# Kernel tuning notes

Hardware: AMD Instinct MI355X
Metric: run time of the kernel (lower is better)

Reference implementation:

```python
import jax, jax.numpy as jnp
import numpy as np

N_NODES = 100000
N_EDGES = 1600000
IN_FEATS = 128
N_HIDDEN = 128
N_CLASSES = 16
INIT_EPS = 0.0
N_GIN_LAYERS = 4  # n_layers + 1


def setup_inputs() -> dict:
    key = jax.random.key(0)
    ks = jax.random.split(key, 16)
    features = jax.random.normal(ks[0], (N_NODES, IN_FEATS), dtype=jnp.float32)
    src = jax.random.randint(ks[1], (N_EDGES,), 0, N_NODES, dtype=jnp.int64)
    dst = jax.random.randint(ks[2], (N_EDGES,), 0, N_NODES, dtype=jnp.int64)
    def linear(k, fin, fout):
        bound = 1.0 / np.sqrt(fin)
        kw, kb = jax.random.split(k)
        W = jax.random.uniform(kw, (fin, fout), jnp.float32, -bound, bound)
        b = jax.random.uniform(kb, (fout,), jnp.float32, -bound, bound)
        return W, b
    W0, b0 = linear(ks[3], IN_FEATS, N_HIDDEN)
    W1, b1 = linear(ks[4], N_HIDDEN, N_HIDDEN)
    W2, b2 = linear(ks[5], N_HIDDEN, N_HIDDEN)
    W3, b3 = linear(ks[6], N_HIDDEN, N_CLASSES)
    eps = jnp.full((N_GIN_LAYERS,), INIT_EPS, dtype=jnp.float32)
    return {"features": features, "src": src, "dst": dst,
            "W0": W0, "b0": b0, "W1": W1, "b1": b1,
            "W2": W2, "b2": b2, "W3": W3, "b3": b3, "eps": eps}


def _mean_agg(h, src, dst, inv_deg):
    # gather neighbor features along edges, sum into dst, divide by in-degree
    agg = jax.ops.segment_sum(h[src], dst, num_segments=N_NODES)
    return agg * inv_deg


def _gin_layer(h, src, dst, inv_deg, eps, W, b, relu):
    z = (1.0 + eps) * h + _mean_agg(h, src, dst, inv_deg)
    out = z @ W + b  # Dropout is identity in eval mode
    return jax.nn.relu(out) if relu else out


def reference(features, src, dst, W0, b0, W1, b1, W2, b2, W3, b3, eps):
    deg = jax.ops.segment_sum(jnp.ones((src.shape[0],), features.dtype), dst,
                              num_segments=N_NODES)
    inv_deg = (1.0 / jnp.maximum(deg, 1.0))[:, None]
    h = _gin_layer(features, src, dst, inv_deg, eps[0], W0, b0, relu=True)
    h = _gin_layer(h, src, dst, inv_deg, eps[1], W1, b1, relu=True)
    h = _gin_layer(h, src, dst, inv_deg, eps[2], W2, b2, relu=True)
    h = _gin_layer(h, src, dst, inv_deg, eps[3], W3, b3, relu=False)
    return h
```

## Files before the change

### kernel.cpp

```cpp
#include <hip/hip_runtime.h>

#define NODES 100000
#define EDGES 1600000
#define FEATS 128
#define NCLS  16

#define BSH    6
#define BNODES 64
#define NB     ((NODES + BNODES - 1) / BNODES)
#define CHUNK  8192
#define NBLK   ((EDGES + CHUNK - 1) / CHUNK)
#define NHIST  (NB * NBLK)
#define BCAP   2048
#define NGRP   ((NODES + 15) / 16)

typedef unsigned int  u32;
typedef unsigned short u16;
typedef unsigned long long u64;
typedef __attribute__((ext_vector_type(8))) short short8;
typedef __attribute__((ext_vector_type(4))) float f32x4;

__device__ __forceinline__ float b2f(u16 v){ return __uint_as_float(((u32)v)<<16); }
__device__ __forceinline__ u16 f2b(float f){
  u32 u = __float_as_uint(f);
  u += 0x7fffu + ((u>>16)&1u);
  return (u16)(u>>16);
}
__device__ __forceinline__ float blo(u32 p){ return __uint_as_float(p<<16); }
__device__ __forceinline__ float bhi(u32 p){ return __uint_as_float(p & 0xffff0000u); }

__device__ __forceinline__ void gload16(const u16* g, u16* l){
  __builtin_amdgcn_global_load_lds(
      (const __attribute__((address_space(1))) u32*)g,
      (__attribute__((address_space(3))) u32*)l, 16, 0, 0);
}


__global__ __launch_bounds__(256) void pA_k(const int* __restrict__ dst,
                                            int* __restrict__ gh, int E){
  __shared__ int hist[NB];
  int t = threadIdx.x, blk = blockIdx.x;
  for (int j = t; j < NB; j += 256) hist[j] = 0;
  __syncthreads();
  int e0 = blk*CHUNK, e1 = e0 + CHUNK; if (e1 > E) e1 = E;
  for (int e = e0 + t; e < e1; e += 256) atomicAdd(&hist[dst[e] >> BSH], 1);
  __syncthreads();
  for (int j = t; j < NB; j += 256) gh[j*NBLK + blk] = hist[j];
}


__global__ __launch_bounds__(256) void scan1_k(const int* __restrict__ in, int* __restrict__ out,
                                               int* __restrict__ bsum, int n){
  __shared__ int sh[256];
  int t = threadIdx.x;
  int base = blockIdx.x*2048 + t*8;
  int v[8]; int s = 0;
  #pragma unroll
  for (int j=0;j<8;++j) v[j] = (base+j < n) ? in[base+j] : 0;
  #pragma unroll
  for (int j=0;j<8;++j){ int tmp = v[j]; v[j] = s; s += tmp; }
  sh[t] = s; __syncthreads();
  for (int off=1; off<256; off<<=1){
    int x = (t>=off) ? sh[t-off] : 0;
    __syncthreads();
    sh[t] += x;
    __syncthreads();
  }
  int excl = sh[t] - s;
  #pragma unroll
  for (int j=0;j<8;++j) if (base+j < n) out[base+j] = excl + v[j];
  if (t == 255) bsum[blockIdx.x] = sh[255];
}

__global__ __launch_bounds__(256) void scan2_k(const int* __restrict__ bsum,
                                               int* __restrict__ boff, int nb){
  __shared__ int sh[256];
  int t = threadIdx.x;
  int v = (t < nb) ? bsum[t] : 0;
  sh[t] = v; __syncthreads();
  for (int off=1; off<256; off<<=1){
    int x = (t>=off) ? sh[t-off] : 0;
    __syncthreads();
    sh[t] += x;
    __syncthreads();
  }
  if (t < nb) boff[t] = sh[t] - v;
}

__global__ void scan3_k(int* __restrict__ gscan, const int* __restrict__ boff,
                        int* __restrict__ bstart, int n){
  int i = blockIdx.x*256 + threadIdx.x;
  if (i < n){
    int v = gscan[i] + boff[i>>11];
    gscan[i] = v;
    if (i % NBLK == 0) bstart[i / NBLK] = v;
    if (i == 0) bstart[NB] = EDGES;
  }
}


__global__ __launch_bounds__(256) void pC_k(const int* __restrict__ src,
    const int* __restrict__ dst, const int* __restrict__ gscan,
    u32* __restrict__ elist, int E){
  __shared__ int A[NB];
  __shared__ int B[NB];
  __shared__ int sp[256];
  __shared__ u32 pay[CHUNK];
  __shared__ u16 bkt[CHUNK];
  int t = threadIdx.x, blk = blockIdx.x;
  for (int j = t; j < NB; j += 256) A[j] = 0;
  __syncthreads();
  int e0 = blk*CHUNK, e1 = e0 + CHUNK; if (e1 > E) e1 = E;
  int cnt = e1 - e0;
  for (int e = e0 + t; e < e1; e += 256) atomicAdd(&A[dst[e] >> BSH], 1);
  __syncthreads();
  {
    int base = t*7;
    int cv[7]; int s = 0;
    #pragma unroll
    for (int j=0;j<7;++j){ int idx = base+j; cv[j] = (idx < NB) ? A[idx] : 0; s += cv[j]; }
    sp[t] = s; __syncthreads();
    for (int off=1; off<256; off<<=1){
      int x = (t>=off) ? sp[t-off] : 0;
      __syncthreads();
      sp[t] += x;
      __syncthreads();
    }
    int run = sp[t] - s;
    #pragma unroll
    for (int j=0;j<7;++j){
      int idx = base+j;
      if (idx < NB){ A[idx] = run; B[idx] = run; run += cv[j]; }
    }
  }
  __syncthreads();
  for (int j = t; j < NB; j += 256) A[j] = gscan[j*NBLK + blk] - A[j];
  __syncthreads();
  for (int e = e0 + t; e < e1; e += 256){
    int d = dst[e];
    int b = d >> BSH;
    u32 w = ((u32)(d & (BNODES-1)) << 17) | (u32)src[e];
    int r = atomicAdd(&B[b], 1);
    pay[r] = w; bkt[r] = (u16)b;
  }
  __syncthreads();
  for (int i = t; i < cnt; i += 256){
    int b = bkt[i];
    elist[i + A[b]] = pay[i];
  }
}


__global__ __launch_bounds__(256) void csr_k(u32* __restrict__ elist,
    const int* __restrict__ bstart, int* __restrict__ offs, int* __restrict__ degs,
    float* __restrict__ invd, int M){
  __shared__ int hist[BNODES];
  __shared__ int pos[BNODES];
  __shared__ u32 buf[BCAP];
  __shared__ u32 buf2[BCAP];
  int b = blockIdx.x, t = threadIdx.x;
  if (b == 0 && t == 0) offs[M] = EDGES;
  if (t < BNODES) hist[t] = 0;
  __syncthreads();
  int s0 = bstart[b];
  int cnt = bstart[b+1] - s0; if (cnt > BCAP) cnt = BCAP;
  u32* el = elist + s0;
  for (int e = t; e < cnt; e += 256){
    u32 w = el[e];
    buf[e] = w;
    atomicAdd(&hist[w>>17], 1);
  }
  __syncthreads();
  if (t < BNODES){
    int v = hist[t];
    int s = v;
    for (int off = 1; off < BNODES; off <<= 1){
      int x = __shfl_up(s, off);
      if (t >= off) s += x;
    }
    int excl = s - v;
    pos[t] = excl;
    int node = b*BNODES + t;
    if (node < M){
      offs[node] = s0 + excl;
      degs[node] = v;
      invd[node] = 1.f / fmaxf((float)v, 1.f);
    }
  }
  __syncthreads();
  for (int e = t; e < cnt; e += 256){
    u32 w = buf[e];
    int p = atomicAdd(&pos[w>>17], 1);
    buf2[p] = w;
  }
  __syncthreads();
  for (int e = t; e < cnt; e += 256) el[e] = buf2[e];
}


__global__ void convf_k(const float* __restrict__ in, u16* __restrict__ o, int n4){
  int i = blockIdx.x*256 + threadIdx.x;
  if (i < n4){
    float4 x = ((const float4*)in)[i];
    ushort4 r;
    r.x = f2b(x.x); r.y = f2b(x.y); r.z = f2b(x.z); r.w = f2b(x.w);
    ((ushort4*)o)[i] = r;
  }
}

__global__ void convw_k(const float* __restrict__ W, u16* __restrict__ Wt, int Kd, int Nd){
  int i = blockIdx.x*256 + threadIdx.x;
  if (i < Kd*Nd){
    int k = i / Nd, nn = i - k*Nd;
    Wt[nn*Kd + k] = f2b(W[i]);
  }
}


template<int NT>
__global__ __launch_bounds__(256) void gemm_k(const u16* __restrict__ h,
                                              const u16* __restrict__ Wt,
                                              u16* __restrict__ y, int M){
  const int K = FEATS;
  const int N = NT*16;
  int lane = threadIdx.x & 63;
  int wave = threadIdx.x >> 6;
  int m    = lane & 15;
  int quad = lane >> 4;
  int row0 = (blockIdx.x*4 + wave)*16;
  if (row0 >= M) return;
  int rowA = row0 + m; if (rowA > M-1) rowA = M-1;
  const u16* pa = h + (size_t)rowA*K + quad*8;

  f32x4 acc[NT];
  #pragma unroll
  for (int j=0;j<NT;++j) acc[j] = (f32x4){0.f,0.f,0.f,0.f};

  #pragma unroll
  for (int kk=0; kk<K; kk+=32){
    short8 a = *(const short8*)(pa + kk);
    #pragma unroll
    for (int j=0;j<NT;++j){
      short8 b = *(const short8*)(Wt + (size_t)(j*16 + m)*K + kk + quad*8);
      acc[j] = __builtin_amdgcn_mfma_f32_16x16x32_bf16(a, b, acc[j], 0, 0, 0);
    }
  }

  #pragma unroll
  for (int j=0;j<NT;++j){
    #pragma unroll
    for (int r=0;r<4;++r){
      int row = row0 + quad*4 + r;
      if (row < M) y[(size_t)row*N + j*16 + m] = f2b(acc[j][r]);
    }
  }
}


#define TRRD(dstv, lit) asm volatile("ds_read_b64_tr_b16 %0, %1 offset:" lit \
                                     : "=v"(dstv) : "v"(trb2))

__global__ __launch_bounds__(256) void aggM_k(const u16* __restrict__ y,
    const u32* __restrict__ el, const int* __restrict__ offs,
    const float* __restrict__ invd, const float* __restrict__ bias,
    const float* __restrict__ epsv, int ei, u16* __restrict__ hout){
  __shared__ __align__(128) u16 ybuf[4][4096];
  int lane = threadIdx.x & 63;
  int wave = threadIdx.x >> 6;
  int grp = blockIdx.x*4 + wave;
  if (grp >= NGRP) return;
  int v0 = grp << 4;
  int m    = lane & 15;
  int quad = lane >> 4;
  u32 tgt = (u32)(((grp & 3) << 4) + m);

  u16* lb = &ybuf[wave][0];
  typedef __attribute__((address_space(3))) u16 lds_u16;
  u32 lbaddr = (u32)(size_t)(lds_u16*)lb;
  u32 trb2 = lbaddr + (u32)(quad*2048) + (u32)(m*8);

  int rsel = (lane & 7) >> 1;
  int gcol = ((lane >> 3) << 4) + ((lane & 1) << 3);

  int e0 = offs[v0];
  int e1 = offs[v0 + 16];
  int nstep = (e1 - e0 + 31) >> 5;

  f32x4 acc[8];
  #pragma unroll
  for (int cb=0;cb<8;++cb) acc[cb] = (f32x4){0.f,0.f,0.f,0.f};

  for (int st = 0; st < nstep; ++st){
    int idx = e0 + (st<<5) + (lane & 31);
    u32 w = (idx < e1) ? el[idx] : 0xFFFE0000u;

    #pragma unroll
    for (int i=0;i<8;++i){
      u32 ws = (u32)__shfl((int)w, 4*i + rsel);
      int srow = (int)(ws & 0x1FFFFu);
      gload16(y + ((size_t)srow << 7) + gcol, lb + i*512);
    }

    union { u32 wv[4]; short8 s; } au;
    #pragma unroll
    for (int p=0;p<4;++p){
      u32 w0 = (u32)__shfl((int)w, quad*8 + 2*p);
      u32 w1 = (u32)__shfl((int)w, quad*8 + 2*p + 1);
      au.wv[p] = (((w0>>17) == tgt) ? 0x3F80u : 0u)
               | (((w1>>17) == tgt) ? 0x3F800000u : 0u);
    }

    asm volatile("s_waitcnt vmcnt(0)" ::: "memory");
    __builtin_amdgcn_sched_barrier(0);

    u64 t[16];
    TRRD(t[0],  "0");    TRRD(t[1],  "1024");
    TRRD(t[2],  "128");  TRRD(t[3],  "1152");
    TRRD(t[4],  "256");  TRRD(t[5],  "1280");
    TRRD(t[6],  "384");  TRRD(t[7],  "1408");
    TRRD(t[8],  "512");  TRRD(t[9],  "1536");
    TRRD(t[10], "640");  TRRD(t[11], "1664");
    TRRD(t[12], "768");  TRRD(t[13], "1792");
    TRRD(t[14], "896");  TRRD(t[15], "1920");
    asm volatile("s_waitcnt lgkmcnt(0)" ::: "memory");
    __builtin_amdgcn_sched_barrier(0);

    #pragma unroll
    for (int cb=0;cb<8;++cb){
      union { u64 d[2]; short8 s; } bu;
      bu.d[0] = t[2*cb]; bu.d[1] = t[2*cb+1];
      acc[cb] = __builtin_amdgcn_mfma_f32_16x16x32_bf16(au.s, bu.s, acc[cb], 0, 0, 0);
    }
  }

  float myinv = invd[v0 + m];
  float invr[4];
  #pragma unroll
  for (int r=0;r<4;++r) invr[r] = __shfl(myinv, quad*4 + r);
  float e1s = 1.f + epsv[ei];
  #pragma unroll
  for (int cb=0;cb<8;++cb){
    float bi = bias[cb*16 + m];
    #pragma unroll
    for (int r=0;r<4;++r){
      size_t off = (size_t)(v0 + quad*4 + r)*FEATS + cb*16 + m;
      float self = b2f(y[off]);
      float o = fmaxf(e1s*self + invr[r]*acc[cb][r] + bi, 0.f);
      hout[off] = f2b(o);
    }
  }
}


__global__ __launch_bounds__(256) void aggF2_k(const u16* __restrict__ y,
    const u32* __restrict__ el, const int* __restrict__ offs,
    const int* __restrict__ degs, const float* __restrict__ invd,
    const float* __restrict__ bias, const float* __restrict__ epsv,
    float* __restrict__ out, int M){
  int lane = threadIdx.x & 63;
  int v = blockIdx.x*4 + (threadIdx.x >> 6);
  if (v >= M) return;
  int sub = lane >> 3;
  int f2  = lane & 7;
  const u32* y2 = (const u32*)y;
  int start = offs[v], deg = degs[v];
  float acc0 = 0.f, acc1 = 0.f;
  for (int e = sub; e < deg; e += 8){
    u32 s = el[start + e] & 0x1FFFFu;
    u32 p = y2[(size_t)s*8 + f2];
    acc0 += blo(p); acc1 += bhi(p);
  }
  acc0 += __shfl_xor(acc0, 8);  acc1 += __shfl_xor(acc1, 8);
  acc0 += __shfl_xor(acc0, 16); acc1 += __shfl_xor(acc1, 16);
  acc0 += __shfl_xor(acc0, 32); acc1 += __shfl_xor(acc1, 32);
  if (sub == 0){
    u32 pv = y2[(size_t)v*8 + f2];
    float2 bi = ((const float2*)bias)[f2];
    float e1s = 1.f + epsv[3];
    float inv = invd[v];
    out[(size_t)v*NCLS + 2*f2    ] = e1s*blo(pv) + inv*acc0 + bi.x;
    out[(size_t)v*NCLS + 2*f2 + 1] = e1s*bhi(pv) + inv*acc1 + bi.y;
  }
}


extern "C" void kernel_launch(void* const* d_in, const int* in_sizes, int n_in,
                              void* d_out, int out_size, void* d_ws, size_t ws_size,
                              hipStream_t stream){
  const float* feats = (const float*)d_in[0];
  const int*   src   = (const int*)d_in[1];
  const int*   dst   = (const int*)d_in[2];
  const float* W0 = (const float*)d_in[3];  const float* b0 = (const float*)d_in[4];
  const float* W1 = (const float*)d_in[5];  const float* b1 = (const float*)d_in[6];
  const float* W2 = (const float*)d_in[7];  const float* b2 = (const float*)d_in[8];
  const float* W3 = (const float*)d_in[9];  const float* b3 = (const float*)d_in[10];
  const float* eps = (const float*)d_in[11];

  char* w = (char*)d_ws;
  auto alloc = [&](size_t bytes)->char*{
    char* p = w; w += (bytes + 255) & ~(size_t)255; return p;
  };
  int*  gh    = (int*)alloc(sizeof(int)*NHIST);
  int*  gscan = (int*)alloc(sizeof(int)*NHIST);
  int*  bsum  = (int*)alloc(sizeof(int)*256);
  int*  boff  = (int*)alloc(sizeof(int)*256);
  int*  bstart= (int*)alloc(sizeof(int)*(NB+1));
  int*  offs  = (int*)alloc(sizeof(int)*(NODES+1));
  int*  degs  = (int*)alloc(sizeof(int)*NODES);
  float* invd = (float*)alloc(sizeof(float)*NODES);
  u32*  elist = (u32*)alloc(sizeof(u32)*EDGES);
  u16*  hb    = (u16*)alloc(sizeof(u16)*(size_t)NODES*FEATS);
  u16*  yb    = (u16*)alloc(sizeof(u16)*(size_t)NODES*FEATS);
  u16*  Wt0   = (u16*)alloc(sizeof(u16)*128*128);
  u16*  Wt1   = (u16*)alloc(sizeof(u16)*128*128);
  u16*  Wt2   = (u16*)alloc(sizeof(u16)*128*128);
  u16*  Wt3   = (u16*)alloc(sizeof(u16)*16*128);

  pA_k<<<NBLK, 256, 0, stream>>>(dst, gh, EDGES);
  int snb = (NHIST + 2047)/2048;
  scan1_k<<<snb, 256, 0, stream>>>(gh, gscan, bsum, NHIST);
  scan2_k<<<1, 256, 0, stream>>>(bsum, boff, snb);
  scan3_k<<<(NHIST+255)/256, 256, 0, stream>>>(gscan, boff, bstart, NHIST);
  pC_k<<<NBLK, 256, 0, stream>>>(src, dst, gscan, elist, EDGES);
  csr_k<<<NB, 256, 0, stream>>>(elist, bstart, offs, degs, invd, NODES);

  convf_k<<<((NODES*FEATS/4)+255)/256, 256, 0, stream>>>(feats, hb, NODES*FEATS/4);
  convw_k<<<(128*128+255)/256, 256, 0, stream>>>(W0, Wt0, 128, 128);
  convw_k<<<(128*128+255)/256, 256, 0, stream>>>(W1, Wt1, 128, 128);
  convw_k<<<(128*128+255)/256, 256, 0, stream>>>(W2, Wt2, 128, 128);
  convw_k<<<(128*16 +255)/256, 256, 0, stream>>>(W3, Wt3, 128, 16);

  int gblocks = (NODES + 63)/64;
  int mblocks = (NGRP + 3)/4;
  int ablocks = (NODES + 3)/4;

  gemm_k<8><<<gblocks, 256, 0, stream>>>(hb, Wt0, yb, NODES);
  aggM_k<<<mblocks, 256, 0, stream>>>(yb, elist, offs, invd, b0, eps, 0, hb);
  gemm_k<8><<<gblocks, 256, 0, stream>>>(hb, Wt1, yb, NODES);
  aggM_k<<<mblocks, 256, 0, stream>>>(yb, elist, offs, invd, b1, eps, 1, hb);
  gemm_k<8><<<gblocks, 256, 0, stream>>>(hb, Wt2, yb, NODES);
  aggM_k<<<mblocks, 256, 0, stream>>>(yb, elist, offs, invd, b2, eps, 2, hb);

  gemm_k<1><<<gblocks, 256, 0, stream>>>(hb, Wt3, yb, NODES);
  aggF2_k<<<ablocks, 256, 0, stream>>>(yb, elist, offs, degs, invd, b3, eps, (float*)d_out, NODES);
}
```

Before: 505.3 us.

## Double-buffer LDS gathers and prefetch edge lists in aggregation kernel

The neighbor-row gathers into LDS are double-buffered, so step st+1's row loads are issued before step st's transpose reads and MFMAs, and the edge-list word is prefetched two steps ahead with explicit vmcnt waits. This is meant to hide global gather latency behind the MFMA work instead of draining all loads every step. In exchange it doubles LDS per wave (affecting occupancy), relies on hand-counted vmcnt values matching the issued loads, and clamps prefetch indices to stay in bounds.

```diff
diff --git a/kernel.cpp b/kernel.cpp
--- a/kernel.cpp
+++ b/kernel.cpp
@@ -258,13 +258,13 @@
 
 
 #define TRRD(dstv, lit) asm volatile("ds_read_b64_tr_b16 %0, %1 offset:" lit \
-                                     : "=v"(dstv) : "v"(trb2))
+                                     : "=v"(dstv) : "v"(trb_i))
 
 __global__ __launch_bounds__(256) void aggM_k(const u16* __restrict__ y,
     const u32* __restrict__ el, const int* __restrict__ offs,
     const float* __restrict__ invd, const float* __restrict__ bias,
     const float* __restrict__ epsv, int ei, u16* __restrict__ hout){
-  __shared__ __align__(128) u16 ybuf[4][4096];
+  __shared__ __align__(128) u16 ybuf[4][2][4096];
   int lane = threadIdx.x & 63;
   int wave = threadIdx.x >> 6;
   int grp = blockIdx.x*4 + wave;
@@ -272,12 +272,13 @@
   int v0 = grp << 4;
   int m    = lane & 15;
   int quad = lane >> 4;
+  int li   = lane & 31;
   u32 tgt = (u32)(((grp & 3) << 4) + m);
 
-  u16* lb = &ybuf[wave][0];
+  u16* lb0 = &ybuf[wave][0][0];
   typedef __attribute__((address_space(3))) u16 lds_u16;
-  u32 lbaddr = (u32)(size_t)(lds_u16*)lb;
-  u32 trb2 = lbaddr + (u32)(quad*2048) + (u32)(m*8);
+  u32 lbaddr = (u32)(size_t)(lds_u16*)lb0;
+  u32 trb0 = lbaddr + (u32)(quad*2048) + (u32)(m*8);
 
   int rsel = (lane & 7) >> 1;
   int gcol = ((lane >> 3) << 4) + ((lane & 1) << 3);
@@ -290,29 +291,52 @@
   #pragma unroll
   for (int cb=0;cb<8;++cb) acc[cb] = (f32x4){0.f,0.f,0.f,0.f};
 
+  auto elp = [&](int st)->const u32*{
+    int idx = e0 + (st<<5) + li;
+    if (idx > EDGES-1) idx = EDGES-1;
+    return el + idx;
+  };
+  auto maskw = [&](u32 v, int st)->u32{
+    int idx = e0 + (st<<5) + li;
+    return (idx < e1) ? v : 0xFFFE0000u;
+  };
+  auto gathers = [&](u32 wm, u16* dstbuf){
+    #pragma unroll
+    for (int i=0;i<8;++i){
+      u32 ws = (u32)__shfl((int)wm, 4*i + rsel);
+      int srow = (int)(ws & 0x1FFFFu);
+      gload16(y + ((size_t)srow << 7) + gcol, dstbuf + i*512);
+    }
+  };
+
+  u32 v0w;
+  asm volatile("global_load_dword %0, %1, off" : "=v"(v0w) : "v"(elp(0)));
+  asm volatile("s_waitcnt vmcnt(0)" : "+v"(v0w) :: "memory");
+  u32 wcur = maskw(v0w, 0);
+  u32 vnext;
+  asm volatile("global_load_dword %0, %1, off" : "=v"(vnext) : "v"(elp(1)));
+  gathers(wcur, lb0);
+
   for (int st = 0; st < nstep; ++st){
-    int idx = e0 + (st<<5) + (lane & 31);
-    u32 w = (idx < e1) ? el[idx] : 0xFFFE0000u;
-
-    #pragma unroll
-    for (int i=0;i<8;++i){
-      u32 ws = (u32)__shfl((int)w, 4*i + rsel);
-      int srow = (int)(ws & 0x1FFFFu);
-      gload16(y + ((size_t)srow << 7) + gcol, lb + i*512);
-    }
+    asm volatile("s_waitcnt vmcnt(8)" : "+v"(vnext) :: "memory");
+    u32 wn = maskw(vnext, st+1);
+    u32 vfut;
+    asm volatile("global_load_dword %0, %1, off" : "=v"(vfut) : "v"(elp(st+2)));
+    gathers(wn, lb0 + (((st+1)&1) << 12));
 
     union { u32 wv[4]; short8 s; } au;
     #pragma unroll
     for (int p=0;p<4;++p){
-      u32 w0 = (u32)__shfl((int)w, quad*8 + 2*p);
-      u32 w1 = (u32)__shfl((int)w, quad*8 + 2*p + 1);
+      u32 w0 = (u32)__shfl((int)wcur, quad*8 + 2*p);
+      u32 w1 = (u32)__shfl((int)wcur, quad*8 + 2*p + 1);
       au.wv[p] = (((w0>>17) == tgt) ? 0x3F80u : 0u)
                | (((w1>>17) == tgt) ? 0x3F800000u : 0u);
     }
 
-    asm volatile("s_waitcnt vmcnt(0)" ::: "memory");
+    asm volatile("s_waitcnt vmcnt(9)" ::: "memory");
     __builtin_amdgcn_sched_barrier(0);
 
+    u32 trb_i = trb0 + (u32)((st&1) << 13);
     u64 t[16];
     TRRD(t[0],  "0");    TRRD(t[1],  "1024");
     TRRD(t[2],  "128");  TRRD(t[3],  "1152");
@@ -331,7 +355,10 @@
       bu.d[0] = t[2*cb]; bu.d[1] = t[2*cb+1];
       acc[cb] = __builtin_amdgcn_mfma_f32_16x16x32_bf16(au.s, bu.s, acc[cb], 0, 0, 0);
     }
-  }
+
+    wcur = wn; vnext = vfut;
+  }
+  asm volatile("s_waitcnt vmcnt(0)" ::: "memory");
 
   float myinv = invd[v0 + m];
   float invr[4];
```

Result: no change. 499.2 us (-1.2%).
